# Kernel optimization log

Hardware: AMD Instinct MI355X
Metric: run time of the kernel (lower is better)

Reference implementation:

```python
import jax, jax.numpy as jnp
import numpy as np


def setup_inputs() -> dict:
    key = jax.random.key(0)
    ks = jax.random.split(key, 8)
    B, T, H, Hu = 128, 64, 1024, 512
    MJW = 64                    # max_jump_width
    J = 2 * MJW + 1             # size_jump_width_set_nn = 129
    N = 2 * T                   # HMM states (word states + null states)
    I = 64                      # source sentence length
    sc = 0.02
    return {
        "y_hidden": jax.random.normal(ks[0], (B, T, H), jnp.float32),
        # emission probs p(source word i | state s), strictly positive for log
        "emission": jax.random.uniform(ks[1], (B, N, I), jnp.float32, 1e-4, 1.0),
        "source_lengths": jax.random.randint(ks[2], (B,), 1, I + 1),
        "W1": jax.random.normal(ks[3], (H, Hu), jnp.float32) * sc,
        "b1": jnp.zeros((Hu,), jnp.float32),
        "W2": jax.random.normal(ks[4], (Hu, J), jnp.float32) * sc,
        "b2": jnp.zeros((J,), jnp.float32),
        "W3": jax.random.normal(ks[5], (Hu, 1), jnp.float32) * sc,
        "b3": jnp.zeros((1,), jnp.float32),
        "max_jump_width": MJW,
    }


def _build_transition(y_hidden, W1, b1, W2, b2, W3, b3, mjw):
    # Dense(tanh) -> Dense softmax jump-width distribution + Dense sigmoid p0
    B, T, _ = y_hidden.shape
    ts = jnp.tanh(y_hidden @ W1 + b1)                       # [B,T,Hu]
    jw = jax.nn.softmax(ts @ W2 + b2, axis=-1)              # [B,T,J]
    p0 = jax.nn.sigmoid(jnp.squeeze(ts @ W3 + b3, -1))      # [B,T]
    r = jnp.arange(T)
    # banded gather: transition[i, j] = jw[i, mjw + j - i]
    band_idx = mjw + r[None, :] - r[:, None]                # [T,T], in [0, J)
    band = jnp.take_along_axis(jw, band_idx[None], axis=2)  # [B,T,T]
    diag_p0 = jnp.eye(T, dtype=jw.dtype) * p0[:, :, None]   # [B,T,T]
    top = jnp.concatenate([band, diag_p0], axis=2)          # [B,T,2T]
    return jnp.concatenate([top, top], axis=1)              # [B,2T,2T]


def _forward_alignment(transition, emission, source_lengths):
    # Faithful translation of the tf.scan forward algorithm. tf.scan with no
    # initializer uses elems[0] as the initial accumulator and emits it as
    # output[0] (log part = ones, so the [0,0] element is 1.0).
    B, N, I = emission.shape
    em = jnp.transpose(emission, (2, 0, 1))                 # [I,B,N]
    alpha0 = jnp.broadcast_to(em[0][:, None, :], (B, N, N)) # rows all equal e_0
    L0 = jnp.ones((B,), emission.dtype)

    def step(carry, e):
        alpha, L = carry                                    # [B,N,N], [B]
        yi = e[:, None, :]                                  # rows of yi_prob identical
        m1 = jnp.matmul(alpha, transition)                  # [B,N,N]
        tmp = m1 * yi
        tmp = tmp / jnp.sum(tmp, axis=2, keepdims=True)     # row-normalized alpha
        m2 = jnp.matmul(transition, alpha) * yi             # [B,N,N]
        max_j = jnp.max(m2, axis=-1)[:, 0]                  # gather row 0 -> [B]
        state_prev = jnp.sum(m1, axis=1)                    # [B,N]
        state = jnp.log(e) + jnp.log(state_prev) - max_j[:, None]
        state_log = jnp.log(jnp.sum(jnp.exp(state), axis=-1))
        L_new = L + state_log + max_j                       # [B]
        return (tmp, L_new), L_new

    (_, _), logs = jax.lax.scan(step, (alpha0, L0), em[1:])  # [I-1,B]
    logs = jnp.concatenate([L0[None], logs], axis=0).T       # [B,I]
    idx = (source_lengths - 1)[:, None]
    return jnp.take_along_axis(logs, idx, axis=1)[:, 0]      # [B]


def reference(y_hidden, emission, source_lengths, W1, b1, W2, b2, W3, b3, max_jump_width):
    transition = _build_transition(y_hidden, W1, b1, W2, b2, W3, b3, max_jump_width)
    return _forward_alignment(transition, emission, source_lengths)
```

## Files before the change

kernel.cpp:

```cpp
#include <hip/hip_runtime.h>
#include <hip/hip_bf16.h>

typedef float f32x4 __attribute__((ext_vector_type(4)));
typedef __bf16 bf16x8 __attribute__((ext_vector_type(8)));
typedef unsigned short u16;

#define OFF_W1T  0u
#define OFF_W23B 1048576u
#define OFF_TS   1196032u
#define OFF_JWT  9584640u
#define OFF_P0   11681792u

static __device__ __forceinline__ u16 f2bf(float x) {
    __bf16 h = (__bf16)x;
    return __builtin_bit_cast(u16, h);
}

__device__ __forceinline__ void gload16(const void* g, void* l) {
    __builtin_amdgcn_global_load_lds(
        (const __attribute__((address_space(1))) void*)g,
        (__attribute__((address_space(3))) void*)l,
        16, 0, 0);
}

__global__ __launch_bounds__(256) void prep_kernel(
    const float* __restrict__ W1, const float* __restrict__ W2,
    const float* __restrict__ W3,
    __bf16* __restrict__ W1T, __bf16* __restrict__ W23B)
{
    const int t = threadIdx.x;
    if (blockIdx.x < 128) {
        __shared__ __bf16 lds_t[64][72];
        const int kt = blockIdx.x >> 3, nt = blockIdx.x & 7;
        const int k0 = kt * 64, n0 = nt * 64;
        {
            const int kr = t >> 2, c0 = (t & 3) * 16;
            const float* src = W1 + (size_t)(k0 + kr) * 512 + n0 + c0;
            #pragma unroll
            for (int q = 0; q < 4; ++q) {
                float4 v = *(const float4*)(src + q * 4);
                lds_t[kr][c0 + q * 4 + 0] = (__bf16)v.x;
                lds_t[kr][c0 + q * 4 + 1] = (__bf16)v.y;
                lds_t[kr][c0 + q * 4 + 2] = (__bf16)v.z;
                lds_t[kr][c0 + q * 4 + 3] = (__bf16)v.w;
            }
        }
        __syncthreads();
        {
            const int nr = t >> 2, kc = (t & 3) * 16;
            bf16x8 o0, o1;
            #pragma unroll
            for (int j = 0; j < 8; ++j) o0[j] = lds_t[kc + j][nr];
            #pragma unroll
            for (int j = 0; j < 8; ++j) o1[j] = lds_t[kc + 8 + j][nr];
            __bf16* dst = W1T + (size_t)(n0 + nr) * 1024 + k0 + kc;
            *(bf16x8*)(dst)     = o0;
            *(bf16x8*)(dst + 8) = o1;
        }
    } else {
        int g = (blockIdx.x - 128) * 256 + t;
        if (g < 9216) {
            int n = g >> 6;
            int k8 = (g & 63) * 8;
            bf16x8 v;
            #pragma unroll
            for (int j = 0; j < 8; ++j) {
                int k = k8 + j;
                float x = 0.0f;
                if (n < 129) x = W2[(size_t)k * 129 + n];
                else if (n == 129) x = W3[k];
                v[j] = (__bf16)x;
            }
            int kk = k8 >> 5, lg = (k8 >> 3) & 3, ct = n >> 4, lr = n & 15;
            *(bf16x8*)&W23B[(((size_t)(kk * 9 + ct)) * 64 + lg * 16 + lr) * 8] = v;
        }
    }
}

__global__ __launch_bounds__(256, 2) void gemm1_kernel(
    const float* __restrict__ Y, const __bf16* __restrict__ W1T,
    const float* __restrict__ b1, u16* __restrict__ ts)
{
    __shared__ float  As[5][64 * 32];
    __shared__ __bf16 Bs[5][128 * 32];
    const int tid = threadIdx.x;
    const int m0 = blockIdx.x * 64, n0 = blockIdx.y * 128;
    const int wid = tid >> 6, lane = tid & 63;
    const int wr = wid >> 1, wc = wid & 1;
    const int lr = lane & 15, lg = lane >> 4;

    const int al = lane >> 3;
    const int au = (lane & 7) ^ al;
    const float* yA0 = Y + (size_t)(m0 + (wid * 2 + 0) * 8 + al) * 1024 + au * 4;
    const float* yA1 = Y + (size_t)(m0 + (wid * 2 + 1) * 8 + al) * 1024 + au * 4;
    const int bl = lane >> 2;
    const int bu = (lane & 3) ^ ((bl >> 1) & 3);
    const __bf16* wB0 = W1T + (size_t)(n0 + (wid * 2 + 0) * 16 + bl) * 1024 + bu * 8;
    const __bf16* wB1 = W1T + (size_t)(n0 + (wid * 2 + 1) * 16 + bl) * 1024 + bu * 8;

    f32x4 acc[2][4];
    #pragma unroll
    for (int m = 0; m < 2; m++)
        #pragma unroll
        for (int n = 0; n < 4; n++) { f32x4 z = {0.f,0.f,0.f,0.f}; acc[m][n] = z; }

#define STAGE(buf, kt) do { \
    gload16(yA0 + (kt) * 32, &As[buf][(wid * 2 + 0) * 256]); \
    gload16(yA1 + (kt) * 32, &As[buf][(wid * 2 + 1) * 256]); \
    gload16(wB0 + (kt) * 32, &Bs[buf][(wid * 2 + 0) * 512]); \
    gload16(wB1 + (kt) * 32, &Bs[buf][(wid * 2 + 1) * 512]); \
} while (0)

#define COMPUTE(buf) do { \
    bf16x8 af[2]; bf16x8 bfr[4]; \
    _Pragma("unroll") \
    for (int m = 0; m < 2; ++m) { \
        const int row = wr * 32 + m * 16 + lr; \
        const int r7 = row & 7; \
        float4 h0 = *(const float4*)&As[buf][row * 32 + (((lg * 2 + 0) ^ r7) * 4)]; \
        float4 h1 = *(const float4*)&As[buf][row * 32 + (((lg * 2 + 1) ^ r7) * 4)]; \
        bf16x8 tt; \
        tt[0]=(__bf16)h0.x; tt[1]=(__bf16)h0.y; tt[2]=(__bf16)h0.z; tt[3]=(__bf16)h0.w; \
        tt[4]=(__bf16)h1.x; tt[5]=(__bf16)h1.y; tt[6]=(__bf16)h1.z; tt[7]=(__bf16)h1.w; \
        af[m] = tt; \
    } \
    _Pragma("unroll") \
    for (int n = 0; n < 4; ++n) { \
        const int rowb = wc * 64 + n * 16 + lr; \
        bfr[n] = *(const bf16x8*)&Bs[buf][rowb * 32 + ((lg ^ ((rowb >> 1) & 3)) * 8)]; \
    } \
    __builtin_amdgcn_s_setprio(1); \
    _Pragma("unroll") \
    for (int m = 0; m < 2; ++m) \
        _Pragma("unroll") \
        for (int n = 0; n < 4; ++n) \
            acc[m][n] = __builtin_amdgcn_mfma_f32_16x16x32_bf16(af[m], bfr[n], acc[m][n], 0, 0, 0); \
    __builtin_amdgcn_s_setprio(0); \
} while (0)

    STAGE(0, 0); STAGE(1, 1); STAGE(2, 2); STAGE(3, 3);
    {
        int buf = 0, sbuf = 4;
        #pragma unroll 1
        for (int kt = 0; kt < 28; ++kt) {
            asm volatile("s_waitcnt vmcnt(12)" ::: "memory");
            __builtin_amdgcn_s_barrier();
            COMPUTE(buf);
            STAGE(sbuf, kt + 4);
            buf  = (buf  == 4) ? 0 : buf  + 1;
            sbuf = (sbuf == 4) ? 0 : sbuf + 1;
        }
    }
    asm volatile("s_waitcnt vmcnt(12)" ::: "memory");
    __builtin_amdgcn_s_barrier();
    COMPUTE(3);
    asm volatile("s_waitcnt vmcnt(8)" ::: "memory");
    __builtin_amdgcn_s_barrier();
    COMPUTE(4);
    asm volatile("s_waitcnt vmcnt(4)" ::: "memory");
    __builtin_amdgcn_s_barrier();
    COMPUTE(0);
    asm volatile("s_waitcnt vmcnt(0)" ::: "memory");
    __builtin_amdgcn_s_barrier();
    COMPUTE(1);

    #pragma unroll
    for (int m = 0; m < 2; m++) {
        #pragma unroll
        for (int n = 0; n < 4; n++) {
            int col = n0 + wc * 64 + n * 16 + lr;
            float bias = b1[col];
            #pragma unroll
            for (int j = 0; j < 4; j++) {
                int row = m0 + wr * 32 + m * 16 + lg * 4 + j;
                float v = tanhf(acc[m][n][j] + bias);
                ts[(size_t)row * 512 + col] = f2bf(v);
            }
        }
    }
#undef STAGE
#undef COMPUTE
}

__global__ __launch_bounds__(256) void band_kernel(
    const u16* __restrict__ ts, const u16* __restrict__ W23B,
    const float* __restrict__ b2, const float* __restrict__ b3,
    float* __restrict__ jwT, float* __restrict__ p0)
{
    const int b = blockIdx.x;
    const int tid = threadIdx.x;
    const int w = tid >> 6, lane = tid & 63;
    const int lr = lane & 15, lg = lane >> 4;
    const int r0 = b * 64 + w * 16;

    f32x4 acc[9];
    #pragma unroll
    for (int ct = 0; ct < 9; ct++) { f32x4 z = {0.f,0.f,0.f,0.f}; acc[ct] = z; }

    #pragma unroll 4
    for (int kk = 0; kk < 16; ++kk) {
        bf16x8 a = *(const bf16x8*)(ts + (size_t)(r0 + lr) * 512 + kk * 32 + lg * 8);
        #pragma unroll
        for (int ct = 0; ct < 9; ct++) {
            bf16x8 bv = *(const bf16x8*)(W23B + ((size_t)(kk * 9 + ct) * 64 + lane) * 8);
            acc[ct] = __builtin_amdgcn_mfma_f32_16x16x32_bf16(a, bv, acc[ct], 0, 0, 0);
        }
    }

    float b3v = b3[0];
    #pragma unroll
    for (int j = 0; j < 4; j++) {
        int rloc = w * 16 + lg * 4 + j;
        float v[9];
        float mx = -1e30f;
        #pragma unroll
        for (int ct = 0; ct < 9; ct++) {
            int col = ct * 16 + lr;
            if (col < 129) { float x = acc[ct][j] + b2[col]; v[ct] = x; mx = fmaxf(mx, x); }
            else v[ct] = -1e30f;
        }
        #pragma unroll
        for (int o = 1; o < 16; o <<= 1) mx = fmaxf(mx, __shfl_xor(mx, o));
        float sum = 0.f;
        #pragma unroll
        for (int ct = 0; ct < 9; ct++) {
            int col = ct * 16 + lr;
            if (col < 129) { float e = expf(v[ct] - mx); v[ct] = e; sum += e; }
        }
        #pragma unroll
        for (int o = 1; o < 16; o <<= 1) sum += __shfl_xor(sum, o);
        float inv = 1.0f / sum;
        #pragma unroll
        for (int ct = 0; ct < 9; ct++) {
            int col = ct * 16 + lr;
            int cc = col - 64 + rloc;
            if (col < 129 && cc >= 0 && cc < 64)
                jwT[((size_t)b * 64 + cc) * 64 + rloc] = v[ct] * inv;
        }
        if (lr == 1) {
            float pv = acc[8][j] + b3v;
            p0[b * 64 + rloc] = 1.0f / (1.0f + expf(-pv));
        }
    }
}

__global__ __launch_bounds__(64, 1) void recur_kernel(
    const float* __restrict__ jwT, const float* __restrict__ p0g,
    const float* __restrict__ em, const int* __restrict__ slen,
    float* __restrict__ out)
{
    __shared__ float em_s[128][65];
    __shared__ f32x4 a_bc4[16];
    const int b = blockIdx.x, c = threadIdx.x;

    const float* bb = jwT + ((size_t)b * 64 + c) * 64;
    f32x4 B0  = *(const f32x4*)(bb + 0);
    f32x4 B1  = *(const f32x4*)(bb + 4);
    f32x4 B2  = *(const f32x4*)(bb + 8);
    f32x4 B3  = *(const f32x4*)(bb + 12);
    f32x4 B4  = *(const f32x4*)(bb + 16);
    f32x4 B5  = *(const f32x4*)(bb + 20);
    f32x4 B6  = *(const f32x4*)(bb + 24);
    f32x4 B7  = *(const f32x4*)(bb + 28);
    f32x4 B8  = *(const f32x4*)(bb + 32);
    f32x4 B9  = *(const f32x4*)(bb + 36);
    f32x4 B10 = *(const f32x4*)(bb + 40);
    f32x4 B11 = *(const f32x4*)(bb + 44);
    f32x4 B12 = *(const f32x4*)(bb + 48);
    f32x4 B13 = *(const f32x4*)(bb + 52);
    f32x4 B14 = *(const f32x4*)(bb + 56);
    f32x4 B15 = *(const f32x4*)(bb + 60);

    {
        const float4* eg = (const float4*)(em + (size_t)b * 8192);
        #pragma unroll 8
        for (int q = 0; q < 32; ++q) {
            int i4 = c + q * 64;
            float4 v = eg[i4];
            int base = i4 * 4; int n = base >> 6; int ii = base & 63;
            em_s[n][ii] = v.x; em_s[n][ii + 1] = v.y; em_s[n][ii + 2] = v.z; em_s[n][ii + 3] = v.w;
        }
    }
    const float p0r = p0g[b * 64 + c];
    const int idx = slen[b] - 1;
    __syncthreads();

    float ut = em_s[c][0] + em_s[c + 64][0];
    int Eacc = 0;

    unsigned rbase = (unsigned)(uintptr_t)(__attribute__((address_space(3))) void*)&a_bc4[0];
    unsigned waddr = rbase + (unsigned)c * 4u;

    float em_lo = em_s[c][1];
    float em_hi = em_s[c + 64][1];

    #pragma unroll 1
    for (int i = 1; i <= idx; ++i) {
        float aloc = ut;
        f32x4 A0,A1,A2,A3,A4,A5,A6,A7,A8,A9,A10,A11,A12,A13,A14,A15;
        asm volatile(
            "ds_write_b32 %17, %16\n\t"
            "ds_read_b128 %0, %18 offset:0\n\t"
            "ds_read_b128 %1, %18 offset:16\n\t"
            "ds_read_b128 %2, %18 offset:32\n\t"
            "ds_read_b128 %3, %18 offset:48\n\t"
            "ds_read_b128 %4, %18 offset:64\n\t"
            "ds_read_b128 %5, %18 offset:80\n\t"
            "ds_read_b128 %6, %18 offset:96\n\t"
            "ds_read_b128 %7, %18 offset:112\n\t"
            "ds_read_b128 %8, %18 offset:128\n\t"
            "ds_read_b128 %9, %18 offset:144\n\t"
            "ds_read_b128 %10, %18 offset:160\n\t"
            "ds_read_b128 %11, %18 offset:176\n\t"
            "ds_read_b128 %12, %18 offset:192\n\t"
            "ds_read_b128 %13, %18 offset:208\n\t"
            "ds_read_b128 %14, %18 offset:224\n\t"
            "ds_read_b128 %15, %18 offset:240\n\t"
            "s_waitcnt lgkmcnt(0)"
            : "=&v"(A0), "=&v"(A1), "=&v"(A2),  "=&v"(A3),
              "=&v"(A4), "=&v"(A5), "=&v"(A6),  "=&v"(A7),
              "=&v"(A8), "=&v"(A9), "=&v"(A10), "=&v"(A11),
              "=&v"(A12),"=&v"(A13),"=&v"(A14), "=&v"(A15)
            : "v"(ut), "v"(waddr), "v"(rbase)
            : "memory");
        float nlo = em_s[c][i + 1];
        float nhi = em_s[c + 64][i + 1];
        float s0 = 0.f, s1 = 0.f, s2 = 0.f, s3 = 0.f;
        float s4 = 0.f, s5 = 0.f, s6 = 0.f, s7 = 0.f;
#define ACC8(AV, BV, CV, DV) do { \
        s0 = fmaf((AV)[0], (BV)[0], s0); \
        s1 = fmaf((AV)[1], (BV)[1], s1); \
        s2 = fmaf((AV)[2], (BV)[2], s2); \
        s3 = fmaf((AV)[3], (BV)[3], s3); \
        s4 = fmaf((CV)[0], (DV)[0], s4); \
        s5 = fmaf((CV)[1], (DV)[1], s5); \
        s6 = fmaf((CV)[2], (DV)[2], s6); \
        s7 = fmaf((CV)[3], (DV)[3], s7); \
} while (0)
        ACC8(A0, B0,  A1, B1);   ACC8(A2, B2,  A3, B3);
        ACC8(A4, B4,  A5, B5);   ACC8(A6, B6,  A7, B7);
        ACC8(A8, B8,  A9, B9);   ACC8(A10, B10, A11, B11);
        ACC8(A12, B12, A13, B13); ACC8(A14, B14, A15, B15);
#undef ACC8
        float sum = ((s0 + s1) + (s2 + s3)) + ((s4 + s5) + (s6 + s7));
        ut = sum * em_lo + aloc * p0r * em_hi;
        int bits = __builtin_amdgcn_readfirstlane(__float_as_int(ut));
        int ef = (bits >> 23) & 255;
        Eacc += ef - 127;
        ut *= __int_as_float((254 - ef) << 23);
        em_lo = nlo; em_hi = nhi;
    }
    float r = ut;
    #pragma unroll
    for (int o = 1; o < 64; o <<= 1) r += __shfl_xor(r, o);
    if (c == 0) {
        float res = 1.0f;
        if (idx > 0)
            res = 1.0f + 0.6931471805599453f * ((float)Eacc + __log2f(r) + 7.0f * (float)idx);
        out[b] = res;
    }
}

extern "C" void kernel_launch(void* const* d_in, const int* in_sizes, int n_in,
                              void* d_out, int out_size, void* d_ws, size_t ws_size,
                              hipStream_t stream)
{
    const float* Y   = (const float*)d_in[0];
    const float* em  = (const float*)d_in[1];
    const int*   sl  = (const int*)d_in[2];
    const float* W1  = (const float*)d_in[3];
    const float* b1  = (const float*)d_in[4];
    const float* W2  = (const float*)d_in[5];
    const float* b2  = (const float*)d_in[6];
    const float* W3  = (const float*)d_in[7];
    const float* b3  = (const float*)d_in[8];
    float* out = (float*)d_out;
    char* ws = (char*)d_ws;

    __bf16* W1T  = (__bf16*)(ws + OFF_W1T);
    __bf16* W23B = (__bf16*)(ws + OFF_W23B);
    u16*    ts   = (u16*)(ws + OFF_TS);
    float*  jwT  = (float*)(ws + OFF_JWT);
    float*  p0   = (float*)(ws + OFF_P0);

    prep_kernel<<<164, 256, 0, stream>>>(W1, W2, W3, W1T, W23B);
    dim3 g1(128, 4);
    gemm1_kernel<<<g1, 256, 0, stream>>>(Y, W1T, b1, ts);
    band_kernel<<<128, 256, 0, stream>>>(ts, (const u16*)W23B, b2, b3, jwT, p0);
    recur_kernel<<<128, 64, 0, stream>>>(jwT, p0, em, sl, out);
}
```

Before: 81.06 us.

## Remap GEMM blocks per XCD and overlap rescale math with LDS reads in recurrence

The GEMM grid becomes a flat 1D launch whose block index is remapped so that neighbouring row blocks and all four column tiles of a row land on the same XCD, aiming for better L2 reuse of Y and W1T. In the serial recurrence loop, the exponent extraction and rescale factor are now computed from the previous state while the LDS reads are still in flight. The scale is folded into the emission multipliers, and the 8-way scalar FMA chains become packed vector multiply-adds. This shortens the per-step critical path but changes the floating-point summation order.

Result: faster. 76.91 us (-5.1%).

```diff
diff --git a/kernel.cpp b/kernel.cpp
--- a/kernel.cpp
+++ b/kernel.cpp
@@ -84,7 +84,16 @@
     __shared__ float  As[5][64 * 32];
     __shared__ __bf16 Bs[5][128 * 32];
     const int tid = threadIdx.x;
-    const int m0 = blockIdx.x * 64, n0 = blockIdx.y * 128;
+
+    const int bid = blockIdx.x;
+    const int half = bid >> 8;
+    const int b8 = bid & 255;
+    const int xcd = b8 & 7;
+    const int ii = b8 >> 3;
+    const int rb = half * 64 + xcd * 8 + (ii >> 2);
+    const int tb = ii & 3;
+    const int m0 = rb * 64, n0 = tb * 128;
+
     const int wid = tid >> 6, lane = tid & 63;
     const int wr = wid >> 1, wc = wid & 1;
     const int lr = lane & 15, lg = lane >> 4;
@@ -296,7 +305,6 @@
 
     #pragma unroll 1
     for (int i = 1; i <= idx; ++i) {
-        float aloc = ut;
         f32x4 A0,A1,A2,A3,A4,A5,A6,A7,A8,A9,A10,A11,A12,A13,A14,A15;
         asm volatile(
             "ds_write_b32 %17, %16\n\t"
@@ -315,40 +323,36 @@
             "ds_read_b128 %12, %18 offset:192\n\t"
             "ds_read_b128 %13, %18 offset:208\n\t"
             "ds_read_b128 %14, %18 offset:224\n\t"
-            "ds_read_b128 %15, %18 offset:240\n\t"
-            "s_waitcnt lgkmcnt(0)"
+            "ds_read_b128 %15, %18 offset:240"
             : "=&v"(A0), "=&v"(A1), "=&v"(A2),  "=&v"(A3),
               "=&v"(A4), "=&v"(A5), "=&v"(A6),  "=&v"(A7),
               "=&v"(A8), "=&v"(A9), "=&v"(A10), "=&v"(A11),
               "=&v"(A12),"=&v"(A13),"=&v"(A14), "=&v"(A15)
             : "v"(ut), "v"(waddr), "v"(rbase)
             : "memory");
-        float nlo = em_s[c][i + 1];
-        float nhi = em_s[c + 64][i + 1];
-        float s0 = 0.f, s1 = 0.f, s2 = 0.f, s3 = 0.f;
-        float s4 = 0.f, s5 = 0.f, s6 = 0.f, s7 = 0.f;
-#define ACC8(AV, BV, CV, DV) do { \
-        s0 = fmaf((AV)[0], (BV)[0], s0); \
-        s1 = fmaf((AV)[1], (BV)[1], s1); \
-        s2 = fmaf((AV)[2], (BV)[2], s2); \
-        s3 = fmaf((AV)[3], (BV)[3], s3); \
-        s4 = fmaf((CV)[0], (DV)[0], s4); \
-        s5 = fmaf((CV)[1], (DV)[1], s5); \
-        s6 = fmaf((CV)[2], (DV)[2], s6); \
-        s7 = fmaf((CV)[3], (DV)[3], s7); \
-} while (0)
-        ACC8(A0, B0,  A1, B1);   ACC8(A2, B2,  A3, B3);
-        ACC8(A4, B4,  A5, B5);   ACC8(A6, B6,  A7, B7);
-        ACC8(A8, B8,  A9, B9);   ACC8(A10, B10, A11, B11);
-        ACC8(A12, B12, A13, B13); ACC8(A14, B14, A15, B15);
-#undef ACC8
-        float sum = ((s0 + s1) + (s2 + s3)) + ((s4 + s5) + (s6 + s7));
-        ut = sum * em_lo + aloc * p0r * em_hi;
         int bits = __builtin_amdgcn_readfirstlane(__float_as_int(ut));
         int ef = (bits >> 23) & 255;
         Eacc += ef - 127;
-        ut *= __int_as_float((254 - ef) << 23);
-        em_lo = nlo; em_hi = nhi;
+        float scale = __int_as_float((254 - ef) << 23);
+        float emlo_eff = em_lo * scale;
+        float emhi_eff = em_hi * p0r * scale;
+        asm volatile("s_waitcnt lgkmcnt(0)" ::: "memory");
+        __builtin_amdgcn_sched_barrier(0);
+        f32x4 va = A0 * B0;
+        f32x4 vb = A1 * B1;
+        f32x4 vc = A2 * B2;
+        f32x4 vd = A3 * B3;
+        va = va + A4 * B4;   vb = vb + A5 * B5;
+        vc = vc + A6 * B6;   vd = vd + A7 * B7;
+        va = va + A8 * B8;   vb = vb + A9 * B9;
+        vc = vc + A10 * B10; vd = vd + A11 * B11;
+        va = va + A12 * B12; vb = vb + A13 * B13;
+        vc = vc + A14 * B14; vd = vd + A15 * B15;
+        f32x4 vs = (va + vb) + (vc + vd);
+        float sum = (vs[0] + vs[1]) + (vs[2] + vs[3]);
+        ut = sum * emlo_eff + ut * emhi_eff;
+        em_lo = em_s[c][i + 1];
+        em_hi = em_s[c + 64][i + 1];
     }
     float r = ut;
     #pragma unroll
@@ -384,8 +388,7 @@
     float*  p0   = (float*)(ws + OFF_P0);
 
     prep_kernel<<<164, 256, 0, stream>>>(W1, W2, W3, W1T, W23B);
-    dim3 g1(128, 4);
-    gemm1_kernel<<<g1, 256, 0, stream>>>(Y, W1T, b1, ts);
+    gemm1_kernel<<<512, 256, 0, stream>>>(Y, W1T, b1, ts);
     band_kernel<<<128, 256, 0, stream>>>(ts, (const u16*)W23B, b2, b3, jwT, p0);
     recur_kernel<<<128, 64, 0, stream>>>(jwT, p0, em, sl, out);
 }
```
